# Optimization experiments

Hardware: AMD Instinct MI355X
Metric: run time of the kernel (lower is better)

Reference implementation:

```python
import jax, jax.numpy as jnp
import numpy as np

N_NODES = 100000
N_EDGES = 1600000
NODE_FEAT_DIM = 140
NUM_OPCODES = 128
EMBED_DIM = 64
HIDDEN = 128
N_LAYERS = 4
LN_EPS = 1e-5


def _layer_norm(x, g, b):
    mu = jnp.mean(x, axis=-1, keepdims=True)
    var = jnp.mean(jnp.square(x - mu), axis=-1, keepdims=True)
    return (x - mu) * jax.lax.rsqrt(var + LN_EPS) * g + b


def setup_inputs() -> dict:
    key = jax.random.key(0)
    ks = jax.random.split(key, 16)
    node_feat = jax.random.normal(ks[0], (N_NODES, NODE_FEAT_DIM), dtype=jnp.float32)
    node_opcode = jax.random.randint(ks[1], (N_NODES,), 0, NUM_OPCODES)
    topo_depth = jax.random.uniform(ks[2], (N_NODES, 1), dtype=jnp.float32)
    edge_index = jax.random.randint(ks[3], (2, N_EDGES), 0, N_NODES)
    in_dim = NODE_FEAT_DIM + EMBED_DIM + 1  # 205
    s_in = 1.0 / np.sqrt(in_dim)
    s_h = 1.0 / np.sqrt(HIDDEN)
    embed = jax.random.normal(ks[4], (NUM_OPCODES, EMBED_DIM), dtype=jnp.float32)
    embed = embed.at[0].set(0.0)  # padding_idx=0
    W_in = jax.random.uniform(ks[5], (in_dim, HIDDEN), minval=-s_in, maxval=s_in, dtype=jnp.float32)
    b_in = jax.random.uniform(ks[6], (HIDDEN,), minval=-s_in, maxval=s_in, dtype=jnp.float32)
    ln0_g = jnp.ones((HIDDEN,), jnp.float32)
    ln0_b = jnp.zeros((HIDDEN,), jnp.float32)
    # SAGEConv per layer: lin_l (neighbors, with bias), lin_r (self, no bias)
    Wl = jax.random.uniform(ks[7], (N_LAYERS, HIDDEN, HIDDEN), minval=-s_h, maxval=s_h, dtype=jnp.float32)
    bl = jax.random.uniform(ks[8], (N_LAYERS, HIDDEN), minval=-s_h, maxval=s_h, dtype=jnp.float32)
    Wr = jax.random.uniform(ks[9], (N_LAYERS, HIDDEN, HIDDEN), minval=-s_h, maxval=s_h, dtype=jnp.float32)
    ln_g = jnp.ones((N_LAYERS, HIDDEN), jnp.float32)
    ln_b = jnp.zeros((N_LAYERS, HIDDEN), jnp.float32)
    return {"node_feat": node_feat, "topo_depth": topo_depth, "embed": embed,
            "W_in": W_in, "b_in": b_in, "ln0_g": ln0_g, "ln0_b": ln0_b,
            "Wl": Wl, "bl": bl, "Wr": Wr, "ln_g": ln_g, "ln_b": ln_b,
            "node_opcode": node_opcode, "edge_index": edge_index}


def reference(node_feat, topo_depth, embed, W_in, b_in, ln0_g, ln0_b,
              Wl, bl, Wr, ln_g, ln_b, node_opcode, edge_index):
    n = node_feat.shape[0]
    op = jnp.clip(node_opcode, 0, embed.shape[0] - 1)
    h = jnp.concatenate([node_feat, embed[op], topo_depth], axis=-1)  # (n, 205)
    # input_proj: Linear -> LayerNorm -> GELU (dropout = eval identity)
    h = jax.nn.gelu(_layer_norm(h @ W_in + b_in, ln0_g, ln0_b), approximate=False)
    src, tgt = edge_index[0], edge_index[1]
    deg = jax.ops.segment_sum(jnp.ones((src.shape[0],), h.dtype), tgt, num_segments=n)
    inv_deg = (1.0 / jnp.maximum(deg, 1.0))[:, None]
    for i in range(N_LAYERS):
        # mean-SAGE: aggregate source features onto targets
        agg = jax.ops.segment_sum(h[src], tgt, num_segments=n) * inv_deg
        out = agg @ Wl[i] + bl[i] + h @ Wr[i]
        h = _layer_norm(h + jax.nn.gelu(out, approximate=False), ln_g[i], ln_b[i])
    return h
```

## Files before the change

### kernel.cpp

```cpp
#include <hip/hip_runtime.h>
#include <cstdint>
#include <cstddef>

#define NN 100000
#define NE 1600000
#define FEAT 140
#define EMB 64
#define HID 128
#define LN_EPS 1e-5f
#define BK_SHIFT 9
#define NBUCK 196
#define MAXSEG 20480

typedef unsigned int uint;
typedef unsigned short ushort;
using short8 = __attribute__((ext_vector_type(8))) short;
using f32x4  = __attribute__((ext_vector_type(4))) float;

__device__ __forceinline__ float gelu_exact(float x) {
    return 0.5f * x * (1.0f + erff(x * 0.70710678118654752440f));
}

__device__ __forceinline__ ushort f2bf(float f) {
    uint u = __float_as_uint(f);
    uint r = (u + 0x7fff + ((u >> 16) & 1)) >> 16;
    return (ushort)r;
}

__device__ __forceinline__ float bf2f(ushort u) {
    return __uint_as_float(((uint)u) << 16);
}

__device__ __forceinline__ float bflo(uint u) {
    return __uint_as_float(u << 16);
}
__device__ __forceinline__ float bfhi(uint u) {
    return __uint_as_float(u & 0xffff0000u);
}

__global__ __launch_bounds__(256) void pack_weights_kernel(
    const float* __restrict__ W_in, const float* __restrict__ Wl,
    const float* __restrict__ Wr,
    ushort* __restrict__ winp, ushort* __restrict__ wcat)
{
    const int tid = blockIdx.x * 256 + threadIdx.x;
    const int NIN = 7 * 8 * 64;
    const int NL  = 8 * 8 * 64;
    if (tid < NIN) {
        const int kk = tid >> 9;
        const int c  = (tid >> 6) & 7;
        const int l  = tid & 63;
        const int kbase = kk * 32 + (l >> 4) * 8;
        const int col = c * 16 + (l & 15);
        short8 v;
        #pragma unroll
        for (int j = 0; j < 8; ++j) {
            const int k = kbase + j;
            v[j] = (k < 205) ? (short)f2bf(W_in[k * 128 + col]) : (short)0;
        }
        *(short8*)(winp + (size_t)tid * 8) = v;
    } else if (tid < NIN + 4 * NL) {
        const int t2 = tid - NIN;
        const int layer = t2 >> 12;
        const int r = t2 & (NL - 1);
        const int kk = r >> 9;
        const int c  = (r >> 6) & 7;
        const int l  = r & 63;
        const int kbase = kk * 32 + (l >> 4) * 8;
        const int col = c * 16 + (l & 15);
        short8 v;
        #pragma unroll
        for (int j = 0; j < 8; ++j) {
            const int k = kbase + j;
            const float x = (k < 128)
                ? Wl[(size_t)layer * 16384 + k * 128 + col]
                : Wr[(size_t)layer * 16384 + (k - 128) * 128 + col];
            v[j] = (short)f2bf(x);
        }
        *(short8*)(wcat + (size_t)t2 * 8) = v;
    }
}

__global__ __launch_bounds__(256) void input_proj_mfma(
    const float* __restrict__ nf, const float* __restrict__ topo,
    const float* __restrict__ embed, const int* __restrict__ opcode,
    const ushort* __restrict__ Wp, const float* __restrict__ b_in,
    const float* __restrict__ g0, const float* __restrict__ b0,
    ushort* __restrict__ hb_out)
{
    __shared__ ushort xs[64 * 232];
    const int t = threadIdx.x;
    const int node0 = blockIdx.x * 64;

    for (int idx = t; idx < 64 * 35; idx += 256) {
        const int row = idx / 35, c = idx - row * 35;
        const int node = min(node0 + row, NN - 1);
        const float4 v = ((const float4*)nf)[(size_t)node * 35 + c];
        ushort* p = &xs[row * 232 + c * 4];
        p[0] = f2bf(v.x); p[1] = f2bf(v.y); p[2] = f2bf(v.z); p[3] = f2bf(v.w);
    }
    for (int idx = t; idx < 64 * 16; idx += 256) {
        const int row = idx >> 4, c = idx & 15;
        const int node = min(node0 + row, NN - 1);
        int op = opcode[node];
        op = min(max(op, 0), 127);
        const float4 v = ((const float4*)embed)[op * 16 + c];
        ushort* p = &xs[row * 232 + 140 + c * 4];
        p[0] = f2bf(v.x); p[1] = f2bf(v.y); p[2] = f2bf(v.z); p[3] = f2bf(v.w);
    }
    if (t < 64) {
        const int node = min(node0 + t, NN - 1);
        xs[t * 232 + 204] = f2bf(topo[node]);
    }
    for (int idx = t; idx < 64 * 19; idx += 256) {
        const int row = idx / 19, c = 205 + (idx - row * 19);
        xs[row * 232 + c] = 0;
    }
    __syncthreads();

    const int w = t >> 6, l = t & 63;
    const int gq = l >> 4, li = l & 15;

    f32x4 acc[8];
    #pragma unroll
    for (int c = 0; c < 8; ++c) acc[c] = (f32x4){0.f, 0.f, 0.f, 0.f};

    const short8* Bp = (const short8*)Wp;
    for (int kk = 0; kk < 7; ++kk) {
        const short8 a = *(const short8*)&xs[(w * 16 + li) * 232 + kk * 32 + gq * 8];
        #pragma unroll
        for (int c = 0; c < 8; ++c) {
            const short8 b = Bp[(kk * 8 + c) * 64 + l];
            acc[c] = __builtin_amdgcn_mfma_f32_16x16x32_bf16(a, b, acc[c], 0, 0, 0);
        }
    }

    float bias[8], gam[8], bet[8];
    #pragma unroll
    for (int c = 0; c < 8; ++c) {
        bias[c] = b_in[c * 16 + li];
        gam[c]  = g0[c * 16 + li];
        bet[c]  = b0[c * 16 + li];
    }
    float s[4] = {0, 0, 0, 0}, q[4] = {0, 0, 0, 0};
    #pragma unroll
    for (int c = 0; c < 8; ++c)
        #pragma unroll
        for (int r = 0; r < 4; ++r) {
            const float u = acc[c][r] + bias[c];
            acc[c][r] = u;
            s[r] += u;
            q[r] += u * u;
        }
    #pragma unroll
    for (int off = 1; off < 16; off <<= 1)
        #pragma unroll
        for (int r = 0; r < 4; ++r) {
            s[r] += __shfl_xor(s[r], off);
            q[r] += __shfl_xor(q[r], off);
        }
    #pragma unroll
    for (int r = 0; r < 4; ++r) {
        const int node = node0 + w * 16 + gq * 4 + r;
        if (node >= NN) continue;
        const float mean = s[r] * (1.0f / HID);
        const float var  = q[r] * (1.0f / HID) - mean * mean;
        const float rstd = rsqrtf(var + LN_EPS);
        #pragma unroll
        for (int c = 0; c < 8; ++c) {
            const float y = gelu_exact((acc[c][r] - mean) * rstd * gam[c] + bet[c]);
            hb_out[(size_t)node * 128 + c * 16 + li] = f2bf(y);
        }
    }
}

__global__ __launch_bounds__(256) void hist_kernel(const int* __restrict__ tgt,
                                                   int* __restrict__ bhist) {
    __shared__ int lh[NBUCK];
    for (int i = threadIdx.x; i < NBUCK; i += 256) lh[i] = 0;
    __syncthreads();
    const int e0 = blockIdx.x * 2048;
    const int eend = min(e0 + 2048, NE);
    for (int e = e0 + threadIdx.x; e < eend; e += 256)
        atomicAdd(&lh[tgt[e] >> BK_SHIFT], 1);
    __syncthreads();
    for (int i = threadIdx.x; i < NBUCK; i += 256)
        if (lh[i]) atomicAdd(&bhist[i], lh[i]);
}

__global__ __launch_bounds__(256) void bucket_scan_kernel(const int* __restrict__ bhist,
                                                          int* __restrict__ bpos,
                                                          int* __restrict__ bcur) {
    __shared__ int s_[256];
    const int t = threadIdx.x;
    int v = (t < NBUCK) ? bhist[t] : 0;
    s_[t] = v;
    __syncthreads();
    for (int off = 1; off < 256; off <<= 1) {
        int u = (t >= off) ? s_[t - off] : 0;
        __syncthreads();
        s_[t] += u;
        __syncthreads();
    }
    if (t < NBUCK) { bpos[t] = s_[t] - v; bcur[t] = s_[t] - v; }
}

__global__ __launch_bounds__(256) void partition_kernel(const int* __restrict__ src,
                                                        const int* __restrict__ tgt,
                                                        int* __restrict__ bcur,
                                                        uint2* __restrict__ pairs) {
    __shared__ int lh[NBUCK];
    __shared__ int gbase[NBUCK];
    for (int i = threadIdx.x; i < NBUCK; i += 256) lh[i] = 0;
    __syncthreads();
    const int e0 = blockIdx.x * 2048;
    const int eend = min(e0 + 2048, NE);
    int myb[8], myr[8], mys[8], myt[8];
    int cnt = 0;
    for (int e = e0 + threadIdx.x; e < eend; e += 256) {
        const int tv = tgt[e];
        const int b = tv >> BK_SHIFT;
        myb[cnt] = b; myt[cnt] = tv; mys[cnt] = src[e];
        myr[cnt] = atomicAdd(&lh[b], 1);
        ++cnt;
    }
    __syncthreads();
    for (int i = threadIdx.x; i < NBUCK; i += 256)
        gbase[i] = lh[i] ? atomicAdd(&bcur[i], lh[i]) : 0;
    __syncthreads();
    for (int i = 0; i < cnt; ++i)
        pairs[gbase[myb[i]] + myr[i]] = make_uint2((uint)myt[i], (uint)mys[i]);
}

__global__ __launch_bounds__(256) void bucket_fill_kernel(const uint2* __restrict__ pairs,
                                                          const int* __restrict__ bpos,
                                                          const int* __restrict__ bhist,
                                                          int* __restrict__ offs,
                                                          float* __restrict__ inv_deg,
                                                          int* __restrict__ csr) {
    __shared__ int cnt[512];
    __shared__ int pref[512];
    __shared__ int ssum[256];
    __shared__ int stage[MAXSEG];
    const int t = threadIdx.x;
    const int b = blockIdx.x;
    const int n0 = b << BK_SHIFT;
    const int nn = min(512, NN - n0);
    const int p0 = bpos[b], pc = bhist[b];

    for (int i = t; i < 512; i += 256) cnt[i] = 0;
    __syncthreads();
    for (int i = t; i < pc; i += 256)
        atomicAdd(&cnt[(int)pairs[p0 + i].x - n0], 1);
    __syncthreads();
    const int a0 = cnt[2 * t], a1 = cnt[2 * t + 1];
    ssum[t] = a0 + a1;
    __syncthreads();
    for (int off = 1; off < 256; off <<= 1) {
        int u = (t >= off) ? ssum[t - off] : 0;
        __syncthreads();
        ssum[t] += u;
        __syncthreads();
    }
    const int ebase = ssum[t] - a0 - a1;
    pref[2 * t] = ebase;
    pref[2 * t + 1] = ebase + a0;
    __syncthreads();
    for (int i = t; i < nn; i += 256) {
        offs[n0 + i] = p0 + pref[i];
        inv_deg[n0 + i] = 1.0f / fmaxf((float)cnt[i], 1.0f);
    }
    if (b == NBUCK - 1 && t == 0) offs[NN] = NE;
    __syncthreads();
    for (int i = t; i < 512; i += 256) cnt[i] = 0;
    __syncthreads();
    if (pc <= MAXSEG) {
        for (int i = t; i < pc; i += 256) {
            const uint2 pr = pairs[p0 + i];
            const int ln = (int)pr.x - n0;
            const int p = atomicAdd(&cnt[ln], 1);
            stage[pref[ln] + p] = (int)pr.y;
        }
        __syncthreads();
        for (int i = t; i < pc; i += 256) csr[p0 + i] = stage[i];
    } else {
        for (int i = t; i < pc; i += 256) {
            const uint2 pr = pairs[p0 + i];
            const int ln = (int)pr.x - n0;
            const int p = atomicAdd(&cnt[ln], 1);
            csr[p0 + pref[ln] + p] = (int)pr.y;
        }
    }
}

__global__ __launch_bounds__(256) void gather_kernel(const ushort* __restrict__ hb,
                                                     const int* __restrict__ csr,
                                                     const int* __restrict__ offs,
                                                     const float* __restrict__ inv_deg,
                                                     ushort* __restrict__ aggb) {
    const int node = blockIdx.x * 4 + (threadIdx.x >> 6);
    const int lane = threadIdx.x & 63;
    if (node >= NN) return;
    const int beg = offs[node];
    const int end = offs[node + 1];
    const uint* hp = (const uint*)hb;
    float ax = 0.0f, ay = 0.0f;
    int j = beg;
    for (; j + 8 <= end; j += 8) {
        int s0 = csr[j + 0], s1 = csr[j + 1], s2 = csr[j + 2], s3 = csr[j + 3];
        int s4 = csr[j + 4], s5 = csr[j + 5], s6 = csr[j + 6], s7 = csr[j + 7];
        uint u0 = hp[(size_t)s0 * 64 + lane];
        uint u1 = hp[(size_t)s1 * 64 + lane];
        uint u2 = hp[(size_t)s2 * 64 + lane];
        uint u3 = hp[(size_t)s3 * 64 + lane];
        uint u4 = hp[(size_t)s4 * 64 + lane];
        uint u5 = hp[(size_t)s5 * 64 + lane];
        uint u6 = hp[(size_t)s6 * 64 + lane];
        uint u7 = hp[(size_t)s7 * 64 + lane];
        float ax0 = bflo(u0) + bflo(u1);
        float ax1 = bflo(u2) + bflo(u3);
        float ax2 = bflo(u4) + bflo(u5);
        float ax3 = bflo(u6) + bflo(u7);
        float ay0 = bfhi(u0) + bfhi(u1);
        float ay1 = bfhi(u2) + bfhi(u3);
        float ay2 = bfhi(u4) + bfhi(u5);
        float ay3 = bfhi(u6) + bfhi(u7);
        ax += (ax0 + ax1) + (ax2 + ax3);
        ay += (ay0 + ay1) + (ay2 + ay3);
    }
    for (; j + 2 <= end; j += 2) {
        int s0 = csr[j + 0], s1 = csr[j + 1];
        uint u0 = hp[(size_t)s0 * 64 + lane];
        uint u1 = hp[(size_t)s1 * 64 + lane];
        ax += bflo(u0) + bflo(u1);
        ay += bfhi(u0) + bfhi(u1);
    }
    if (j < end) {
        uint u0 = hp[(size_t)csr[j] * 64 + lane];
        ax += bflo(u0);
        ay += bfhi(u0);
    }
    const float id = inv_deg[node];
    const uint lo = f2bf(ax * id);
    const uint hi = f2bf(ay * id);
    ((uint*)aggb)[(size_t)node * 64 + lane] = lo | (hi << 16);
}

__global__ __launch_bounds__(256) void layer_mfma(
    ushort* __restrict__ hb, const ushort* __restrict__ aggb,
    const ushort* __restrict__ Wp, const float* __restrict__ bl,
    const float* __restrict__ g, const float* __restrict__ b,
    float* __restrict__ hout, int write_f32)
{
    const int t = threadIdx.x;
    const int w = t >> 6, l = t & 63;
    const int gq = l >> 4, li = l & 15;
    const int node0 = blockIdx.x * 64;
    const int ar = min(node0 + w * 16 + li, NN - 1);

    f32x4 acc[8];
    #pragma unroll
    for (int c = 0; c < 8; ++c) acc[c] = (f32x4){0.f, 0.f, 0.f, 0.f};

    const short8* Bp = (const short8*)Wp;
    const short8* Ag = (const short8*)aggb;
    const short8* Hg = (const short8*)hb;
    #pragma unroll
    for (int kk = 0; kk < 8; ++kk) {
        const short8 a = (kk < 4) ? Ag[(size_t)ar * 16 + kk * 4 + gq]
                                  : Hg[(size_t)ar * 16 + (kk - 4) * 4 + gq];
        #pragma unroll
        for (int c = 0; c < 8; ++c) {
            const short8 bf = Bp[(kk * 8 + c) * 64 + l];
            acc[c] = __builtin_amdgcn_mfma_f32_16x16x32_bf16(a, bf, acc[c], 0, 0, 0);
        }
    }

    float bias[8], gam[8], bet[8];
    #pragma unroll
    for (int c = 0; c < 8; ++c) {
        bias[c] = bl[c * 16 + li];
        gam[c]  = g[c * 16 + li];
        bet[c]  = b[c * 16 + li];
    }
    float s[4] = {0, 0, 0, 0}, q[4] = {0, 0, 0, 0};
    #pragma unroll
    for (int r = 0; r < 4; ++r) {
        const int nd = min(node0 + w * 16 + gq * 4 + r, NN - 1);
        #pragma unroll
        for (int c = 0; c < 8; ++c) {
            const float hv = bf2f(hb[(size_t)nd * 128 + c * 16 + li]);
            const float tv = hv + gelu_exact(acc[c][r] + bias[c]);
            acc[c][r] = tv;
            s[r] += tv;
            q[r] += tv * tv;
        }
    }
    #pragma unroll
    for (int off = 1; off < 16; off <<= 1)
        #pragma unroll
        for (int r = 0; r < 4; ++r) {
            s[r] += __shfl_xor(s[r], off);
            q[r] += __shfl_xor(q[r], off);
        }
    #pragma unroll
    for (int r = 0; r < 4; ++r) {
        const int node = node0 + w * 16 + gq * 4 + r;
        if (node >= NN) continue;
        const float mean = s[r] * (1.0f / HID);
        const float var  = q[r] * (1.0f / HID) - mean * mean;
        const float rstd = rsqrtf(var + LN_EPS);
        #pragma unroll
        for (int c = 0; c < 8; ++c) {
            const float y = (acc[c][r] - mean) * rstd * gam[c] + bet[c];
            hb[(size_t)node * 128 + c * 16 + li] = f2bf(y);
            if (write_f32) hout[(size_t)node * 128 + c * 16 + li] = y;
        }
    }
}

extern "C" void kernel_launch(void* const* d_in, const int* in_sizes, int n_in,
                              void* d_out, int out_size, void* d_ws, size_t ws_size,
                              hipStream_t stream) {
    const float* node_feat = (const float*)d_in[0];
    const float* topo      = (const float*)d_in[1];
    const float* embed     = (const float*)d_in[2];
    const float* W_in      = (const float*)d_in[3];
    const float* b_in      = (const float*)d_in[4];
    const float* ln0_g     = (const float*)d_in[5];
    const float* ln0_b     = (const float*)d_in[6];
    const float* Wl        = (const float*)d_in[7];
    const float* bl        = (const float*)d_in[8];
    const float* Wr        = (const float*)d_in[9];
    const float* ln_g      = (const float*)d_in[10];
    const float* ln_b      = (const float*)d_in[11];
    const int*   opcode    = (const int*)d_in[12];
    const int*   edge      = (const int*)d_in[13];
    const int*   e_src = edge;
    const int*   e_tgt = edge + NE;

    float* h = (float*)d_out;

    char* w = (char*)d_ws;
    ushort* hb     = (ushort*)w;  w += (size_t)NN * HID * sizeof(ushort);
    ushort* aggb   = (ushort*)w;  w += (size_t)NN * HID * sizeof(ushort);
    float* inv_deg = (float*)w;   w += 400016;
    int*   offs    = (int*)w;     w += 400016;
    int*   bhist   = (int*)w;     w += 1024;
    int*   bpos    = (int*)w;     w += 1024;
    int*   bcur    = (int*)w;     w += 1024;
    int*   csr     = (int*)w;     w += (size_t)NE * sizeof(int);
    uint2* pairs   = (uint2*)w;   w += (size_t)NE * sizeof(uint2);
    ushort* winp   = (ushort*)w;  w += 7 * 8 * 64 * 8 * sizeof(ushort);
    ushort* wcat   = (ushort*)w;  w += 4 * 8 * 8 * 64 * 8 * sizeof(ushort);

    const int EBLK = (NE + 2047) / 2048;

    pack_weights_kernel<<<78, 256, 0, stream>>>(W_in, Wl, Wr, winp, wcat);

    input_proj_mfma<<<(NN + 63) / 64, 256, 0, stream>>>(
        node_feat, topo, embed, opcode, winp, b_in, ln0_g, ln0_b, hb);

    hipMemsetAsync(bhist, 0, NBUCK * sizeof(int), stream);
    hist_kernel<<<EBLK, 256, 0, stream>>>(e_tgt, bhist);
    bucket_scan_kernel<<<1, 256, 0, stream>>>(bhist, bpos, bcur);
    partition_kernel<<<EBLK, 256, 0, stream>>>(e_src, e_tgt, bcur, pairs);
    bucket_fill_kernel<<<NBUCK, 256, 0, stream>>>(pairs, bpos, bhist, offs, inv_deg, csr);

    for (int layer = 0; layer < 4; ++layer) {
        gather_kernel<<<NN / 4, 256, 0, stream>>>(hb, csr, offs, inv_deg, aggb);
        layer_mfma<<<(NN + 63) / 64, 256, 0, stream>>>(
            hb, aggb, wcat + (size_t)layer * 8 * 8 * 64 * 8,
            bl + (size_t)layer * HID,
            ln_g + (size_t)layer * HID, ln_b + (size_t)layer * HID,
            h, layer == 3 ? 1 : 0);
    }
}
```

Measured before the change: 576.4 us.

## Fuse neighbor gather into layer MFMA kernel with ping-pong hidden buffers

The separate gather kernel is merged into the per-layer MFMA kernel. Each wave aggregates its 16 nodes' neighbor features into shared memory, and those values feed the MFMA A operand directly. This removes the aggregate buffer's global write and re-read plus one launch per layer. Hidden state now ping-pongs between two buffers to avoid read/write races. The cost is lower gather parallelism: each wave walks 16 nodes serially over 1563 blocks instead of 25000 small blocks, so latency hiding may suffer.

New measurement: 973.2 us. 68.8% more time.

```diff
diff --git a/kernel.cpp b/kernel.cpp
--- a/kernel.cpp
+++ b/kernel.cpp
@@ -293,82 +293,77 @@
     }
 }
 
-__global__ __launch_bounds__(256) void gather_kernel(const ushort* __restrict__ hb,
-                                                     const int* __restrict__ csr,
-                                                     const int* __restrict__ offs,
-                                                     const float* __restrict__ inv_deg,
-                                                     ushort* __restrict__ aggb) {
-    const int node = blockIdx.x * 4 + (threadIdx.x >> 6);
-    const int lane = threadIdx.x & 63;
-    if (node >= NN) return;
-    const int beg = offs[node];
-    const int end = offs[node + 1];
-    const uint* hp = (const uint*)hb;
-    float ax = 0.0f, ay = 0.0f;
-    int j = beg;
-    for (; j + 8 <= end; j += 8) {
-        int s0 = csr[j + 0], s1 = csr[j + 1], s2 = csr[j + 2], s3 = csr[j + 3];
-        int s4 = csr[j + 4], s5 = csr[j + 5], s6 = csr[j + 6], s7 = csr[j + 7];
-        uint u0 = hp[(size_t)s0 * 64 + lane];
-        uint u1 = hp[(size_t)s1 * 64 + lane];
-        uint u2 = hp[(size_t)s2 * 64 + lane];
-        uint u3 = hp[(size_t)s3 * 64 + lane];
-        uint u4 = hp[(size_t)s4 * 64 + lane];
-        uint u5 = hp[(size_t)s5 * 64 + lane];
-        uint u6 = hp[(size_t)s6 * 64 + lane];
-        uint u7 = hp[(size_t)s7 * 64 + lane];
-        float ax0 = bflo(u0) + bflo(u1);
-        float ax1 = bflo(u2) + bflo(u3);
-        float ax2 = bflo(u4) + bflo(u5);
-        float ax3 = bflo(u6) + bflo(u7);
-        float ay0 = bfhi(u0) + bfhi(u1);
-        float ay1 = bfhi(u2) + bfhi(u3);
-        float ay2 = bfhi(u4) + bfhi(u5);
-        float ay3 = bfhi(u6) + bfhi(u7);
-        ax += (ax0 + ax1) + (ax2 + ax3);
-        ay += (ay0 + ay1) + (ay2 + ay3);
-    }
-    for (; j + 2 <= end; j += 2) {
-        int s0 = csr[j + 0], s1 = csr[j + 1];
-        uint u0 = hp[(size_t)s0 * 64 + lane];
-        uint u1 = hp[(size_t)s1 * 64 + lane];
-        ax += bflo(u0) + bflo(u1);
-        ay += bfhi(u0) + bfhi(u1);
-    }
-    if (j < end) {
-        uint u0 = hp[(size_t)csr[j] * 64 + lane];
-        ax += bflo(u0);
-        ay += bfhi(u0);
-    }
-    const float id = inv_deg[node];
-    const uint lo = f2bf(ax * id);
-    const uint hi = f2bf(ay * id);
-    ((uint*)aggb)[(size_t)node * 64 + lane] = lo | (hi << 16);
-}
-
-__global__ __launch_bounds__(256) void layer_mfma(
-    ushort* __restrict__ hb, const ushort* __restrict__ aggb,
+__global__ __launch_bounds__(256) void layer_fused(
+    const ushort* __restrict__ hb_in, ushort* __restrict__ hb_out,
+    const int* __restrict__ csr, const int* __restrict__ offs,
+    const float* __restrict__ inv_deg,
     const ushort* __restrict__ Wp, const float* __restrict__ bl,
     const float* __restrict__ g, const float* __restrict__ b,
     float* __restrict__ hout, int write_f32)
 {
+    __shared__ uint agg_s[64][68];
     const int t = threadIdx.x;
     const int w = t >> 6, l = t & 63;
     const int gq = l >> 4, li = l & 15;
     const int node0 = blockIdx.x * 64;
+    const uint* hp = (const uint*)hb_in;
+
+    for (int n = 0; n < 16; ++n) {
+        const int node = min(node0 + w * 16 + n, NN - 1);
+        const int beg = offs[node];
+        const int end = offs[node + 1];
+        float ax = 0.0f, ay = 0.0f;
+        int j = beg;
+        for (; j + 8 <= end; j += 8) {
+            int s0 = csr[j + 0], s1 = csr[j + 1], s2 = csr[j + 2], s3 = csr[j + 3];
+            int s4 = csr[j + 4], s5 = csr[j + 5], s6 = csr[j + 6], s7 = csr[j + 7];
+            uint u0 = hp[(size_t)s0 * 64 + l];
+            uint u1 = hp[(size_t)s1 * 64 + l];
+            uint u2 = hp[(size_t)s2 * 64 + l];
+            uint u3 = hp[(size_t)s3 * 64 + l];
+            uint u4 = hp[(size_t)s4 * 64 + l];
+            uint u5 = hp[(size_t)s5 * 64 + l];
+            uint u6 = hp[(size_t)s6 * 64 + l];
+            uint u7 = hp[(size_t)s7 * 64 + l];
+            float ax0 = bflo(u0) + bflo(u1);
+            float ax1 = bflo(u2) + bflo(u3);
+            float ax2 = bflo(u4) + bflo(u5);
+            float ax3 = bflo(u6) + bflo(u7);
+            float ay0 = bfhi(u0) + bfhi(u1);
+            float ay1 = bfhi(u2) + bfhi(u3);
+            float ay2 = bfhi(u4) + bfhi(u5);
+            float ay3 = bfhi(u6) + bfhi(u7);
+            ax += (ax0 + ax1) + (ax2 + ax3);
+            ay += (ay0 + ay1) + (ay2 + ay3);
+        }
+        for (; j + 2 <= end; j += 2) {
+            int s0 = csr[j + 0], s1 = csr[j + 1];
+            uint u0 = hp[(size_t)s0 * 64 + l];
+            uint u1 = hp[(size_t)s1 * 64 + l];
+            ax += bflo(u0) + bflo(u1);
+            ay += bfhi(u0) + bfhi(u1);
+        }
+        if (j < end) {
+            uint u0 = hp[(size_t)csr[j] * 64 + l];
+            ax += bflo(u0);
+            ay += bfhi(u0);
+        }
+        const float id = inv_deg[node];
+        agg_s[w * 16 + n][l] = (uint)f2bf(ax * id) | ((uint)f2bf(ay * id) << 16);
+    }
+
     const int ar = min(node0 + w * 16 + li, NN - 1);
-
     f32x4 acc[8];
     #pragma unroll
     for (int c = 0; c < 8; ++c) acc[c] = (f32x4){0.f, 0.f, 0.f, 0.f};
 
     const short8* Bp = (const short8*)Wp;
-    const short8* Ag = (const short8*)aggb;
-    const short8* Hg = (const short8*)hb;
+    const short8* Hg = (const short8*)hb_in;
     #pragma unroll
     for (int kk = 0; kk < 8; ++kk) {
-        const short8 a = (kk < 4) ? Ag[(size_t)ar * 16 + kk * 4 + gq]
-                                  : Hg[(size_t)ar * 16 + (kk - 4) * 4 + gq];
+        const short8 a = (kk < 4)
+            ? *(const short8*)&agg_s[w * 16 + li][kk * 16 + gq * 4]
+            : Hg[(size_t)ar * 16 + (kk - 4) * 4 + gq];
         #pragma unroll
         for (int c = 0; c < 8; ++c) {
             const short8 bf = Bp[(kk * 8 + c) * 64 + l];
@@ -389,7 +384,7 @@
         const int nd = min(node0 + w * 16 + gq * 4 + r, NN - 1);
         #pragma unroll
         for (int c = 0; c < 8; ++c) {
-            const float hv = bf2f(hb[(size_t)nd * 128 + c * 16 + li]);
+            const float hv = bf2f(hb_in[(size_t)nd * 128 + c * 16 + li]);
             const float tv = hv + gelu_exact(acc[c][r] + bias[c]);
             acc[c][r] = tv;
             s[r] += tv;
@@ -413,7 +408,7 @@
         #pragma unroll
         for (int c = 0; c < 8; ++c) {
             const float y = (acc[c][r] - mean) * rstd * gam[c] + bet[c];
-            hb[(size_t)node * 128 + c * 16 + li] = f2bf(y);
+            hb_out[(size_t)node * 128 + c * 16 + li] = f2bf(y);
             if (write_f32) hout[(size_t)node * 128 + c * 16 + li] = y;
         }
     }
@@ -442,8 +437,8 @@
     float* h = (float*)d_out;
 
     char* w = (char*)d_ws;
-    ushort* hb     = (ushort*)w;  w += (size_t)NN * HID * sizeof(ushort);
-    ushort* aggb   = (ushort*)w;  w += (size_t)NN * HID * sizeof(ushort);
+    ushort* hbA    = (ushort*)w;  w += (size_t)NN * HID * sizeof(ushort);
+    ushort* hbB    = (ushort*)w;  w += (size_t)NN * HID * sizeof(ushort);
     float* inv_deg = (float*)w;   w += 400016;
     int*   offs    = (int*)w;     w += 400016;
     int*   bhist   = (int*)w;     w += 1024;
@@ -459,7 +454,7 @@
     pack_weights_kernel<<<78, 256, 0, stream>>>(W_in, Wl, Wr, winp, wcat);
 
     input_proj_mfma<<<(NN + 63) / 64, 256, 0, stream>>>(
-        node_feat, topo, embed, opcode, winp, b_in, ln0_g, ln0_b, hb);
+        node_feat, topo, embed, opcode, winp, b_in, ln0_g, ln0_b, hbA);
 
     hipMemsetAsync(bhist, 0, NBUCK * sizeof(int), stream);
     hist_kernel<<<EBLK, 256, 0, stream>>>(e_tgt, bhist);
@@ -467,12 +462,15 @@
     partition_kernel<<<EBLK, 256, 0, stream>>>(e_src, e_tgt, bcur, pairs);
     bucket_fill_kernel<<<NBUCK, 256, 0, stream>>>(pairs, bpos, bhist, offs, inv_deg, csr);
 
+    ushort* hin = hbA;
+    ushort* hout_b = hbB;
     for (int layer = 0; layer < 4; ++layer) {
-        gather_kernel<<<NN / 4, 256, 0, stream>>>(hb, csr, offs, inv_deg, aggb);
-        layer_mfma<<<(NN + 63) / 64, 256, 0, stream>>>(
-            hb, aggb, wcat + (size_t)layer * 8 * 8 * 64 * 8,
+        layer_fused<<<(NN + 63) / 64, 256, 0, stream>>>(
+            hin, hout_b, csr, offs, inv_deg,
+            wcat + (size_t)layer * 8 * 8 * 64 * 8,
             bl + (size_t)layer * HID,
             ln_g + (size_t)layer * HID, ln_b + (size_t)layer * HID,
             h, layer == 3 ? 1 : 0);
-    }
-}
+        ushort* tmp = hin; hin = hout_b; hout_b = tmp;
+    }
+}
```
